# Performance work log

Hardware: AMD Instinct MI355X
Metric: run time of the kernel (lower is better)

The kernel has to match this reference:

```python
import jax, jax.numpy as jnp
import numpy as np

B, N, D, M = 16, 4096, 640, 64  # D = hidden_dim*2 + u_in = 2*256 + 128


def setup_inputs() -> dict:
    key = jax.random.key(0)
    kx, kk, kv = jax.random.split(key, 3)
    x = jax.random.normal(kx, (B, N, D), dtype=jnp.float32)
    Mk = jax.random.normal(kk, (M, D), dtype=jnp.float32)
    Mv = jax.random.normal(kv, (M, D), dtype=jnp.float32)
    return {"x": x, "Mk": Mk, "Mv": Mv}


def reference(x, Mk, Mv):
    # scores: [B, N, M] = x @ Mk^T
    scores = jnp.einsum('bnd,md->bnm', x, Mk)
    weights = jax.nn.softmax(scores, axis=-1)
    # out: [B, N, D] = weights @ Mv
    out = jnp.einsum('bnm,md->bnd', weights, Mv)
    return out
```

## Files before the change

### kernel.cpp

```cpp
#include <hip/hip_runtime.h>

typedef float  f32x4  __attribute__((ext_vector_type(4)));
typedef short  short8 __attribute__((ext_vector_type(8)));
typedef __bf16 bf16x8 __attribute__((ext_vector_type(8)));

#define DEV static __device__ __forceinline__

DEV f32x4 mfma16(short8 a, short8 b, f32x4 c) {
  return __builtin_amdgcn_mfma_f32_16x16x32_bf16(
      __builtin_bit_cast(bf16x8, a), __builtin_bit_cast(bf16x8, b), c, 0, 0, 0);
}

DEV void splitf(float f, unsigned short& hi, unsigned short& lo) {
  unsigned u = __builtin_bit_cast(unsigned, f);
  hi = (unsigned short)(u >> 16);
  float hf = __builtin_bit_cast(float, u & 0xFFFF0000u);
  float r = f - hf;
  unsigned v = __builtin_bit_cast(unsigned, r);
  lo = (unsigned short)((v + 0x7FFFu + ((v >> 16) & 1u)) >> 16);
}

DEV unsigned short rne16(float f) {
  unsigned v = __builtin_bit_cast(unsigned, f);
  return (unsigned short)((v + 0x7FFFu + ((v >> 16) & 1u)) >> 16);
}

#define DDIM 640
#define KCH  20
#define MKP_ELEMS (KCH*2*4*64*8)
#define MVP_OFF   MKP_ELEMS

__global__ void ea_pack(const float* __restrict__ Mk, const float* __restrict__ Mv,
                        unsigned short* __restrict__ ws) {
  int tid = blockIdx.x * 256 + threadIdx.x;
  unsigned short* MkP = ws;
  unsigned short* MvP = ws + MVP_OFF;
  if (tid < 5120) {
    int c = tid >> 8;
    int g = (tid >> 6) & 3;
    int l = tid & 63;
    int t = l & 15, q = l >> 4;
    const float* src = Mk + (16*g + t) * DDIM + 32*c + 8*q;
    unsigned short* dh = MkP + (((c*2 + 0)*4 + g)*64 + l)*8;
    unsigned short* dl = MkP + (((c*2 + 1)*4 + g)*64 + l)*8;
#pragma unroll
    for (int j = 0; j < 8; ++j) splitf(src[j], dh[j], dl[j]);
  } else if (tid < 10240) {
    int s = tid - 5120;
    int n = s >> 7;
    int c = (s >> 6) & 1;
    int l = s & 63;
    int t = l & 15, q = l >> 4;
    const float* src = Mv + (32*c + 8*q) * DDIM + 16*n + t;
    unsigned short* dh = MvP + ((n*2 + c)*64 + l)*8;
#pragma unroll
    for (int j = 0; j < 8; ++j) dh[j] = rne16(src[j*DDIM]);
  }
}

#define LOADX(X0, X1, c) { X0 = *(const f32x4*)(xp + 32*(c)); \
                           X1 = *(const f32x4*)(xp + 32*(c) + 4); }

#define LOADF(c) { const unsigned short* mkc_ = MkP + (c)*4096 + l*8;        \
  fh0 = *(const short8*)(mkc_);        fh1 = *(const short8*)(mkc_ + 512);   \
  fh2 = *(const short8*)(mkc_ + 1024); fh3 = *(const short8*)(mkc_ + 1536);  \
  fl0 = *(const short8*)(mkc_ + 2048); fl1 = *(const short8*)(mkc_ + 2560);  \
  fl2 = *(const short8*)(mkc_ + 3072); fl3 = *(const short8*)(mkc_ + 3584); }

#define SPLITX(X0, X1)                                                       \
  splitf(X0[0], ah.u[0], al.u[0]); splitf(X0[1], ah.u[1], al.u[1]);          \
  splitf(X0[2], ah.u[2], al.u[2]); splitf(X0[3], ah.u[3], al.u[3]);          \
  splitf(X1[0], ah.u[4], al.u[4]); splitf(X1[1], ah.u[5], al.u[5]);          \
  splitf(X1[2], ah.u[6], al.u[6]); splitf(X1[3], ah.u[7], al.u[7]);

#define MFMAS()                                                              \
  acc[0] = mfma16(ah.s, fh0, acc[0]); acc[1] = mfma16(ah.s, fh1, acc[1]);    \
  acc[2] = mfma16(ah.s, fh2, acc[2]); acc[3] = mfma16(ah.s, fh3, acc[3]);    \
  acc[0] = mfma16(al.s, fh0, acc[0]); acc[1] = mfma16(al.s, fh1, acc[1]);    \
  acc[2] = mfma16(al.s, fh2, acc[2]); acc[3] = mfma16(al.s, fh3, acc[3]);    \
  acc[0] = mfma16(ah.s, fl0, acc[0]); acc[1] = mfma16(ah.s, fl1, acc[1]);    \
  acc[2] = mfma16(ah.s, fl2, acc[2]); acc[3] = mfma16(ah.s, fl3, acc[3]);

__global__ __launch_bounds__(64, 4) void ea_main(const float* __restrict__ x,
                                                 const unsigned short* __restrict__ MkP,
                                                 const unsigned short* __restrict__ MvP,
                                                 float* __restrict__ out) {
  __shared__ __align__(16) unsigned short Wh[16][64];
  __shared__ __align__(16) unsigned short Wl[16][64];
  const int l = threadIdx.x;
  const int t = l & 15;
  const int q = l >> 4;
  const long row0 = (long)blockIdx.x * 16;

  const float* xp = x + (row0 + t) * DDIM + 8*q;
  f32x4 acc[4];
#pragma unroll
  for (int g = 0; g < 4; ++g) acc[g] = (f32x4){0.f, 0.f, 0.f, 0.f};

  f32x4 x00,x01,x10,x11,x20,x21,x30,x31;
  short8 fh0,fh1,fh2,fh3, fl0,fl1,fl2,fl3;
  union { short8 s; unsigned short u[8]; } ah, al;

  LOADX(x00,x01, 0) LOADX(x10,x11, 1) LOADX(x20,x21, 2) LOADX(x30,x31, 3)

#pragma unroll
  for (int cc = 0; cc < KCH; cc += 4) {
    const bool pf = (cc + 4 < KCH);
    LOADF(cc)     SPLITX(x00, x01) if (pf) { LOADX(x00,x01, cc+4) } MFMAS()
    LOADF(cc+1)   SPLITX(x10, x11) if (pf) { LOADX(x10,x11, cc+5) } MFMAS()
    LOADF(cc+2)   SPLITX(x20, x21) if (pf) { LOADX(x20,x21, cc+6) } MFMAS()
    LOADF(cc+3)   SPLITX(x30, x31) if (pf) { LOADX(x30,x31, cc+7) } MFMAS()
  }

  float rmax[4], rsum[4];
#pragma unroll
  for (int j = 0; j < 4; ++j)
    rmax[j] = fmaxf(fmaxf(acc[0][j], acc[1][j]), fmaxf(acc[2][j], acc[3][j]));
#pragma unroll
  for (int mk = 1; mk <= 8; mk <<= 1) {
#pragma unroll
    for (int j = 0; j < 4; ++j)
      rmax[j] = fmaxf(rmax[j], __shfl_xor(rmax[j], mk, 64));
  }
#pragma unroll
  for (int g = 0; g < 4; ++g)
#pragma unroll
    for (int j = 0; j < 4; ++j)
      acc[g][j] = exp2f((acc[g][j] - rmax[j]) * 1.44269504f);
#pragma unroll
  for (int j = 0; j < 4; ++j)
    rsum[j] = (acc[0][j] + acc[1][j]) + (acc[2][j] + acc[3][j]);
#pragma unroll
  for (int mk = 1; mk <= 8; mk <<= 1) {
#pragma unroll
    for (int j = 0; j < 4; ++j)
      rsum[j] += __shfl_xor(rsum[j], mk, 64);
  }
#pragma unroll
  for (int j = 0; j < 4; ++j) rsum[j] = 1.0f / rsum[j];

#pragma unroll
  for (int g = 0; g < 4; ++g)
#pragma unroll
    for (int j = 0; j < 4; ++j) {
      float wt = acc[g][j] * rsum[j];
      unsigned short hi, lo;
      splitf(wt, hi, lo);
      int row = 4*q + j;
      int ms  = (16*g + t) ^ ((row & 7) << 3);
      Wh[row][ms] = hi;
      Wl[row][ms] = lo;
    }
  asm volatile("s_waitcnt lgkmcnt(0)" ::: "memory");
  __builtin_amdgcn_sched_barrier(0);

  short8 aH0, aH1, aL0, aL1;
  {
    const int sw  = (t & 7) << 3;
    const int ms0 = (8*q) ^ sw;
    const int ms1 = (32 + 8*q) ^ sw;
    aH0 = *(const short8*)&Wh[t][ms0];
    aH1 = *(const short8*)&Wh[t][ms1];
    aL0 = *(const short8*)&Wl[t][ms0];
    aL1 = *(const short8*)&Wl[t][ms1];
  }

  short8 vA0, vA1, vB0, vB1;
  {
    const unsigned short* mvp = MvP + l*8;
    vA0 = *(const short8*)(mvp);
    vA1 = *(const short8*)(mvp + 512);
  }
  float* opb = out + (row0 + 4*q) * DDIM + t;

#pragma unroll 2
  for (int n = 0; n < 40; n += 2) {
    {
      const unsigned short* mvp = MvP + (n + 1) * 1024 + l*8;
      vB0 = *(const short8*)(mvp);
      vB1 = *(const short8*)(mvp + 512);
    }
    {
      f32x4 o = (f32x4){0.f,0.f,0.f,0.f};
      o = mfma16(aH0, vA0, o); o = mfma16(aL0, vA0, o);
      o = mfma16(aH1, vA1, o); o = mfma16(aL1, vA1, o);
      float* op = opb + 16*n;
#pragma unroll
      for (int j = 0; j < 4; ++j) __builtin_nontemporal_store(o[j], op + j*DDIM);
    }
    if (n + 2 < 40) {
      const unsigned short* mvp = MvP + (n + 2) * 1024 + l*8;
      vA0 = *(const short8*)(mvp);
      vA1 = *(const short8*)(mvp + 512);
    }
    {
      f32x4 o = (f32x4){0.f,0.f,0.f,0.f};
      o = mfma16(aH0, vB0, o); o = mfma16(aL0, vB0, o);
      o = mfma16(aH1, vB1, o); o = mfma16(aL1, vB1, o);
      float* op = opb + 16*(n + 1);
#pragma unroll
      for (int j = 0; j < 4; ++j) __builtin_nontemporal_store(o[j], op + j*DDIM);
    }
  }
}

extern "C" void kernel_launch(void* const* d_in, const int* in_sizes, int n_in,
                              void* d_out, int out_size, void* d_ws, size_t ws_size,
                              hipStream_t stream) {
  const float* x  = (const float*)d_in[0];
  const float* Mk = (const float*)d_in[1];
  const float* Mv = (const float*)d_in[2];
  float* outp = (float*)d_out;
  unsigned short* ws = (unsigned short*)d_ws;

  ea_pack<<<40, 256, 0, stream>>>(Mk, Mv, ws);
  ea_main<<<4096, 64, 0, stream>>>(x, ws, ws + MVP_OFF, outp);
}
```

Before: 85.25 us.

## Process two 16-row tiles per wave to reuse Mk/Mv fragment loads

Each single-wave block now handles 32 rows instead of 16. Every Mk and Mv fragment load feeds two sets of MFMAs, which halves the global/L2 traffic for the packed weight matrices per row, and the grid shrinks to 2048 blocks. In exchange register pressure roughly doubles, the launch-bounds occupancy hint drops from 4 to 2, and the x prefetch depth goes from 4 chunks to 2 per tile, which may expose more load latency.

Result: slower. 97.12 us (+13.9%).

```diff
diff --git a/kernel.cpp b/kernel.cpp
--- a/kernel.cpp
+++ b/kernel.cpp
@@ -58,8 +58,8 @@
   }
 }
 
-#define LOADX(X0, X1, c) { X0 = *(const f32x4*)(xp + 32*(c)); \
-                           X1 = *(const f32x4*)(xp + 32*(c) + 4); }
+#define LOADXP(X0, X1, xp, c) { X0 = *(const f32x4*)((xp) + 32*(c)); \
+                                X1 = *(const f32x4*)((xp) + 32*(c) + 4); }
 
 #define LOADF(c) { const unsigned short* mkc_ = MkP + (c)*4096 + l*8;        \
   fh0 = *(const short8*)(mkc_);        fh1 = *(const short8*)(mkc_ + 512);   \
@@ -73,96 +73,112 @@
   splitf(X1[0], ah.u[4], al.u[4]); splitf(X1[1], ah.u[5], al.u[5]);          \
   splitf(X1[2], ah.u[6], al.u[6]); splitf(X1[3], ah.u[7], al.u[7]);
 
-#define MFMAS()                                                              \
-  acc[0] = mfma16(ah.s, fh0, acc[0]); acc[1] = mfma16(ah.s, fh1, acc[1]);    \
-  acc[2] = mfma16(ah.s, fh2, acc[2]); acc[3] = mfma16(ah.s, fh3, acc[3]);    \
-  acc[0] = mfma16(al.s, fh0, acc[0]); acc[1] = mfma16(al.s, fh1, acc[1]);    \
-  acc[2] = mfma16(al.s, fh2, acc[2]); acc[3] = mfma16(al.s, fh3, acc[3]);    \
-  acc[0] = mfma16(ah.s, fl0, acc[0]); acc[1] = mfma16(ah.s, fl1, acc[1]);    \
-  acc[2] = mfma16(ah.s, fl2, acc[2]); acc[3] = mfma16(ah.s, fl3, acc[3]);
-
-__global__ __launch_bounds__(64, 4) void ea_main(const float* __restrict__ x,
+#define MFMAS(ACC)                                                           \
+  ACC[0] = mfma16(ah.s, fh0, ACC[0]); ACC[1] = mfma16(ah.s, fh1, ACC[1]);    \
+  ACC[2] = mfma16(ah.s, fh2, ACC[2]); ACC[3] = mfma16(ah.s, fh3, ACC[3]);    \
+  ACC[0] = mfma16(al.s, fh0, ACC[0]); ACC[1] = mfma16(al.s, fh1, ACC[1]);    \
+  ACC[2] = mfma16(al.s, fh2, ACC[2]); ACC[3] = mfma16(al.s, fh3, ACC[3]);    \
+  ACC[0] = mfma16(ah.s, fl0, ACC[0]); ACC[1] = mfma16(ah.s, fl1, ACC[1]);    \
+  ACC[2] = mfma16(ah.s, fl2, ACC[2]); ACC[3] = mfma16(ah.s, fl3, ACC[3]);
+
+#define G1_STEP(c, XA0, XA1, XB0, XB1) {                                     \
+  LOADF(c)                                                                   \
+  SPLITX(XA0, XA1)                                                           \
+  if ((c) + 2 < KCH) { LOADXP(XA0, XA1, xpA, (c)+2) }                        \
+  MFMAS(accA)                                                                \
+  SPLITX(XB0, XB1)                                                           \
+  if ((c) + 2 < KCH) { LOADXP(XB0, XB1, xpB, (c)+2) }                        \
+  MFMAS(accB)                                                                \
+}
+
+#define SOFTMAX_W(ACC, RB) {                                                 \
+  float rmax_[4], rsum_[4];                                                  \
+  _Pragma("unroll")                                                          \
+  for (int j = 0; j < 4; ++j)                                                \
+    rmax_[j] = fmaxf(fmaxf(ACC[0][j], ACC[1][j]), fmaxf(ACC[2][j], ACC[3][j]));\
+  _Pragma("unroll")                                                          \
+  for (int mk = 1; mk <= 8; mk <<= 1) {                                      \
+    _Pragma("unroll")                                                        \
+    for (int j = 0; j < 4; ++j)                                              \
+      rmax_[j] = fmaxf(rmax_[j], __shfl_xor(rmax_[j], mk, 64));              \
+  }                                                                          \
+  _Pragma("unroll")                                                          \
+  for (int g = 0; g < 4; ++g)                                                \
+    _Pragma("unroll")                                                        \
+    for (int j = 0; j < 4; ++j)                                              \
+      ACC[g][j] = exp2f((ACC[g][j] - rmax_[j]) * 1.44269504f);               \
+  _Pragma("unroll")                                                          \
+  for (int j = 0; j < 4; ++j)                                                \
+    rsum_[j] = (ACC[0][j] + ACC[1][j]) + (ACC[2][j] + ACC[3][j]);            \
+  _Pragma("unroll")                                                          \
+  for (int mk = 1; mk <= 8; mk <<= 1) {                                      \
+    _Pragma("unroll")                                                        \
+    for (int j = 0; j < 4; ++j)                                              \
+      rsum_[j] += __shfl_xor(rsum_[j], mk, 64);                              \
+  }                                                                          \
+  _Pragma("unroll")                                                          \
+  for (int j = 0; j < 4; ++j) rsum_[j] = 1.0f / rsum_[j];                    \
+  _Pragma("unroll")                                                          \
+  for (int g = 0; g < 4; ++g)                                                \
+    _Pragma("unroll")                                                        \
+    for (int j = 0; j < 4; ++j) {                                            \
+      float wt = ACC[g][j] * rsum_[j];                                       \
+      unsigned short hi, lo;                                                 \
+      splitf(wt, hi, lo);                                                    \
+      int row = (RB) + 4*q + j;                                              \
+      int ms  = (16*g + t) ^ ((row & 7) << 3);                               \
+      Wh[row][ms] = hi;                                                      \
+      Wl[row][ms] = lo;                                                      \
+    }                                                                        \
+}
+
+__global__ __launch_bounds__(64, 2) void ea_main(const float* __restrict__ x,
                                                  const unsigned short* __restrict__ MkP,
                                                  const unsigned short* __restrict__ MvP,
                                                  float* __restrict__ out) {
-  __shared__ __align__(16) unsigned short Wh[16][64];
-  __shared__ __align__(16) unsigned short Wl[16][64];
+  __shared__ __align__(16) unsigned short Wh[32][64];
+  __shared__ __align__(16) unsigned short Wl[32][64];
   const int l = threadIdx.x;
   const int t = l & 15;
   const int q = l >> 4;
-  const long row0 = (long)blockIdx.x * 16;
-
-  const float* xp = x + (row0 + t) * DDIM + 8*q;
-  f32x4 acc[4];
-#pragma unroll
-  for (int g = 0; g < 4; ++g) acc[g] = (f32x4){0.f, 0.f, 0.f, 0.f};
-
-  f32x4 x00,x01,x10,x11,x20,x21,x30,x31;
+  const long row0 = (long)blockIdx.x * 32;
+
+  const float* xpA = x + (row0 + t) * DDIM + 8*q;
+  const float* xpB = xpA + 16 * DDIM;
+  f32x4 accA[4], accB[4];
+#pragma unroll
+  for (int g = 0; g < 4; ++g) {
+    accA[g] = (f32x4){0.f, 0.f, 0.f, 0.f};
+    accB[g] = (f32x4){0.f, 0.f, 0.f, 0.f};
+  }
+
+  f32x4 xA0,xA1,xA2,xA3, xB0,xB1,xB2,xB3;
   short8 fh0,fh1,fh2,fh3, fl0,fl1,fl2,fl3;
   union { short8 s; unsigned short u[8]; } ah, al;
 
-  LOADX(x00,x01, 0) LOADX(x10,x11, 1) LOADX(x20,x21, 2) LOADX(x30,x31, 3)
-
-#pragma unroll
-  for (int cc = 0; cc < KCH; cc += 4) {
-    const bool pf = (cc + 4 < KCH);
-    LOADF(cc)     SPLITX(x00, x01) if (pf) { LOADX(x00,x01, cc+4) } MFMAS()
-    LOADF(cc+1)   SPLITX(x10, x11) if (pf) { LOADX(x10,x11, cc+5) } MFMAS()
-    LOADF(cc+2)   SPLITX(x20, x21) if (pf) { LOADX(x20,x21, cc+6) } MFMAS()
-    LOADF(cc+3)   SPLITX(x30, x31) if (pf) { LOADX(x30,x31, cc+7) } MFMAS()
-  }
-
-  float rmax[4], rsum[4];
-#pragma unroll
-  for (int j = 0; j < 4; ++j)
-    rmax[j] = fmaxf(fmaxf(acc[0][j], acc[1][j]), fmaxf(acc[2][j], acc[3][j]));
-#pragma unroll
-  for (int mk = 1; mk <= 8; mk <<= 1) {
-#pragma unroll
-    for (int j = 0; j < 4; ++j)
-      rmax[j] = fmaxf(rmax[j], __shfl_xor(rmax[j], mk, 64));
-  }
-#pragma unroll
-  for (int g = 0; g < 4; ++g)
-#pragma unroll
-    for (int j = 0; j < 4; ++j)
-      acc[g][j] = exp2f((acc[g][j] - rmax[j]) * 1.44269504f);
-#pragma unroll
-  for (int j = 0; j < 4; ++j)
-    rsum[j] = (acc[0][j] + acc[1][j]) + (acc[2][j] + acc[3][j]);
-#pragma unroll
-  for (int mk = 1; mk <= 8; mk <<= 1) {
-#pragma unroll
-    for (int j = 0; j < 4; ++j)
-      rsum[j] += __shfl_xor(rsum[j], mk, 64);
-  }
-#pragma unroll
-  for (int j = 0; j < 4; ++j) rsum[j] = 1.0f / rsum[j];
-
-#pragma unroll
-  for (int g = 0; g < 4; ++g)
-#pragma unroll
-    for (int j = 0; j < 4; ++j) {
-      float wt = acc[g][j] * rsum[j];
-      unsigned short hi, lo;
-      splitf(wt, hi, lo);
-      int row = 4*q + j;
-      int ms  = (16*g + t) ^ ((row & 7) << 3);
-      Wh[row][ms] = hi;
-      Wl[row][ms] = lo;
-    }
+  LOADXP(xA0,xA1, xpA, 0) LOADXP(xB0,xB1, xpB, 0)
+  LOADXP(xA2,xA3, xpA, 1) LOADXP(xB2,xB3, xpB, 1)
+
+#pragma unroll
+  for (int cc = 0; cc < KCH; cc += 2) {
+    G1_STEP(cc,   xA0,xA1, xB0,xB1)
+    G1_STEP(cc+1, xA2,xA3, xB2,xB3)
+  }
+
+  SOFTMAX_W(accA, 0)
+  SOFTMAX_W(accB, 16)
   asm volatile("s_waitcnt lgkmcnt(0)" ::: "memory");
   __builtin_amdgcn_sched_barrier(0);
 
-  short8 aH0, aH1, aL0, aL1;
+  short8 aHA0, aHA1, aLA0, aLA1, aHB0, aHB1, aLB0, aLB1;
   {
     const int sw  = (t & 7) << 3;
     const int ms0 = (8*q) ^ sw;
     const int ms1 = (32 + 8*q) ^ sw;
-    aH0 = *(const short8*)&Wh[t][ms0];
-    aH1 = *(const short8*)&Wh[t][ms1];
-    aL0 = *(const short8*)&Wl[t][ms0];
-    aL1 = *(const short8*)&Wl[t][ms1];
+    aHA0 = *(const short8*)&Wh[t][ms0];      aHA1 = *(const short8*)&Wh[t][ms1];
+    aLA0 = *(const short8*)&Wl[t][ms0];      aLA1 = *(const short8*)&Wl[t][ms1];
+    aHB0 = *(const short8*)&Wh[16+t][ms0];   aHB1 = *(const short8*)&Wh[16+t][ms1];
+    aLB0 = *(const short8*)&Wl[16+t][ms0];   aLB1 = *(const short8*)&Wl[16+t][ms1];
   }
 
   short8 vA0, vA1, vB0, vB1;
@@ -171,7 +187,8 @@
     vA0 = *(const short8*)(mvp);
     vA1 = *(const short8*)(mvp + 512);
   }
-  float* opb = out + (row0 + 4*q) * DDIM + t;
+  float* opA = out + (row0 + 4*q) * DDIM + t;
+  float* opB = opA + 16 * DDIM;
 
 #pragma unroll 2
   for (int n = 0; n < 40; n += 2) {
@@ -181,12 +198,19 @@
       vB1 = *(const short8*)(mvp + 512);
     }
     {
-      f32x4 o = (f32x4){0.f,0.f,0.f,0.f};
-      o = mfma16(aH0, vA0, o); o = mfma16(aL0, vA0, o);
-      o = mfma16(aH1, vA1, o); o = mfma16(aL1, vA1, o);
-      float* op = opb + 16*n;
-#pragma unroll
-      for (int j = 0; j < 4; ++j) __builtin_nontemporal_store(o[j], op + j*DDIM);
+      f32x4 oA = (f32x4){0.f,0.f,0.f,0.f};
+      f32x4 oB = (f32x4){0.f,0.f,0.f,0.f};
+      oA = mfma16(aHA0, vA0, oA); oA = mfma16(aLA0, vA0, oA);
+      oA = mfma16(aHA1, vA1, oA); oA = mfma16(aLA1, vA1, oA);
+      oB = mfma16(aHB0, vA0, oB); oB = mfma16(aLB0, vA0, oB);
+      oB = mfma16(aHB1, vA1, oB); oB = mfma16(aLB1, vA1, oB);
+      float* pA = opA + 16*n;
+      float* pB = opB + 16*n;
+#pragma unroll
+      for (int j = 0; j < 4; ++j) {
+        __builtin_nontemporal_store(oA[j], pA + j*DDIM);
+        __builtin_nontemporal_store(oB[j], pB + j*DDIM);
+      }
     }
     if (n + 2 < 40) {
       const unsigned short* mvp = MvP + (n + 2) * 1024 + l*8;
@@ -194,12 +218,19 @@
       vA1 = *(const short8*)(mvp + 512);
     }
     {
-      f32x4 o = (f32x4){0.f,0.f,0.f,0.f};
-      o = mfma16(aH0, vB0, o); o = mfma16(aL0, vB0, o);
-      o = mfma16(aH1, vB1, o); o = mfma16(aL1, vB1, o);
-      float* op = opb + 16*(n + 1);
-#pragma unroll
-      for (int j = 0; j < 4; ++j) __builtin_nontemporal_store(o[j], op + j*DDIM);
+      f32x4 oA = (f32x4){0.f,0.f,0.f,0.f};
+      f32x4 oB = (f32x4){0.f,0.f,0.f,0.f};
+      oA = mfma16(aHA0, vB0, oA); oA = mfma16(aLA0, vB0, oA);
+      oA = mfma16(aHA1, vB1, oA); oA = mfma16(aLA1, vB1, oA);
+      oB = mfma16(aHB0, vB0, oB); oB = mfma16(aLB0, vB0, oB);
+      oB = mfma16(aHB1, vB1, oB); oB = mfma16(aLB1, vB1, oB);
+      float* pA = opA + 16*(n + 1);
+      float* pB = opB + 16*(n + 1);
+#pragma unroll
+      for (int j = 0; j < 4; ++j) {
+        __builtin_nontemporal_store(oA[j], pA + j*DDIM);
+        __builtin_nontemporal_store(oB[j], pB + j*DDIM);
+      }
     }
   }
 }
@@ -214,5 +245,5 @@
   unsigned short* ws = (unsigned short*)d_ws;
 
   ea_pack<<<40, 256, 0, stream>>>(Mk, Mv, ws);
-  ea_main<<<4096, 64, 0, stream>>>(x, ws, ws + MVP_OFF, outp);
-}
+  ea_main<<<2048, 64, 0, stream>>>(x, ws, ws + MVP_OFF, outp);
+}
```
